# Performance work log

Measured on AMD Instinct MI355X. Metric: run time of the kernel, lower is better.

Reference implementation:

```python
import jax, jax.numpy as jnp
import numpy as np

N = 100000   # nodes
E = 1600000  # edges
D = 128      # input_dim
H = 128      # hidden_dim
G = 1000     # num graphs
C = 10       # output_dim
EPS = 1e-5   # BatchNorm eps


def setup_inputs() -> dict:
    key = jax.random.key(0)
    ks = jax.random.split(key, 16)
    inp = {
        "x": jax.random.normal(ks[0], (N, D), dtype=jnp.float32),
        "edge_index": jax.random.randint(ks[1], (2, E), 0, N, dtype=jnp.int64),
        "batch": jnp.sort(jax.random.randint(ks[2], (N,), 0, G, dtype=jnp.int64)),
    }
    s_in, s_h = 1.0 / np.sqrt(D), 1.0 / np.sqrt(H)
    inp["W1"] = jax.random.normal(ks[3], (D, H), jnp.float32) * s_in
    inp["b1"] = jnp.zeros((H,), jnp.float32)
    inp["W2"] = jax.random.normal(ks[4], (H, H), jnp.float32) * s_h
    inp["b2"] = jnp.zeros((H,), jnp.float32)
    inp["W3"] = jax.random.normal(ks[5], (H, H), jnp.float32) * s_h
    inp["b3"] = jnp.zeros((H,), jnp.float32)
    for i in range(1, 4):
        inp[f"g{i}"] = jnp.ones((H,), jnp.float32)
        inp[f"be{i}"] = jnp.zeros((H,), jnp.float32)
    inp["Wc1"] = jax.random.normal(ks[6], (H, H // 2), jnp.float32) * s_h
    inp["bc1"] = jnp.zeros((H // 2,), jnp.float32)
    inp["Wc2"] = jax.random.normal(ks[7], (H // 2, C), jnp.float32) * (1.0 / np.sqrt(H // 2))
    inp["bc2"] = jnp.zeros((C,), jnp.float32)
    return inp


def _edge_norm(edge_index, num_nodes):
    # PyG GCNConv default: add self-loops, symmetric D^-1/2 A D^-1/2 normalization
    loop = jnp.arange(num_nodes, dtype=edge_index.dtype)
    src = jnp.concatenate([edge_index[0], loop])
    dst = jnp.concatenate([edge_index[1], loop])
    deg = jax.ops.segment_sum(jnp.ones_like(dst, dtype=jnp.float32), dst,
                              num_segments=num_nodes)
    dinv = jnp.where(deg > 0, deg ** -0.5, 0.0)
    norm = dinv[src] * dinv[dst]  # [E + N]
    return src, dst, norm


def _gcn_conv(x, W, b, src, dst, norm, num_nodes):
    h = x @ W                              # [N, H]
    msg = h[src] * norm[:, None]           # gather over edges (incl. self-loops)
    out = jax.ops.segment_sum(msg, dst, num_segments=num_nodes)
    return out + b


def _bn_eval(x, gamma, beta):
    # eval-mode BatchNorm1d with running_mean=0, running_var=1 buffers
    return gamma * x * (1.0 / np.sqrt(1.0 + EPS)) + beta


def reference(x, edge_index, batch,
              W1, b1, W2, b2, W3, b3,
              g1, be1, g2, be2, g3, be3,
              Wc1, bc1, Wc2, bc2):
    num_nodes = x.shape[0]
    src, dst, norm = _edge_norm(edge_index, num_nodes)
    h = x
    for (W, b, g, be) in ((W1, b1, g1, be1), (W2, b2, g2, be2), (W3, b3, g3, be3)):
        h = _gcn_conv(h, W, b, src, dst, norm, num_nodes)
        h = jax.nn.relu(_bn_eval(h, g, be))  # dropout is identity in eval mode
    # global_mean_pool over graph ids
    sums = jax.ops.segment_sum(h, batch, num_segments=G)
    cnts = jax.ops.segment_sum(jnp.ones((num_nodes,), h.dtype), batch, num_segments=G)
    pooled = sums / jnp.maximum(cnts, 1.0)[:, None]
    # classifier MLP
    z = jax.nn.relu(pooled @ Wc1 + bc1)
    return z @ Wc2 + bc2
```

## Files before the change

### kernel.cpp

```cpp
#include <hip/hip_runtime.h>
#include <hip/hip_bf16.h>

#define INV1P 0.9999950000374997f
#define BCAP 16384
#define CSRCAP 20480

typedef __attribute__((ext_vector_type(8))) short bfrag;
typedef __attribute__((ext_vector_type(4))) float f32x4;

static __device__ __forceinline__ unsigned bf16rne(float f) {
    unsigned u = __float_as_uint(f);
    return (u + 0x7fffu + ((u >> 16) & 1u)) >> 16;
}
static __device__ __forceinline__ float bflo(unsigned u) { return __uint_as_float(u << 16); }
static __device__ __forceinline__ float bfhi(unsigned u) { return __uint_as_float(u & 0xffff0000u); }


__global__ __launch_bounds__(256) void k_initcur2(int* __restrict__ gcursor) {
    gcursor[threadIdx.x] = threadIdx.x * BCAP;
}

__global__ __launch_bounds__(256) void k_binA(const int* __restrict__ src, const int* __restrict__ dst,
                                              int* __restrict__ gcursor, unsigned* __restrict__ binned, int e) {
    __shared__ unsigned pk[8192];
    __shared__ unsigned char bk[8192];
    __shared__ int hist[256];
    __shared__ int base[256];
    int tid = threadIdx.x;
    hist[tid] = 0;
    __syncthreads();
    int cbase = blockIdx.x * 8192;
    int cnt = min(8192, e - cbase);
    for (int j = tid; j < cnt; j += 256) {
        int s = src[cbase + j], d = dst[cbase + j];
        unsigned b = (unsigned)d >> 9;
        pk[j] = (unsigned)s | (((unsigned)d & 511u) << 17);
        bk[j] = (unsigned char)b;
        atomicAdd(&hist[b], 1);
    }
    __syncthreads();
    int h = hist[tid];
    base[tid] = (h > 0) ? atomicAdd(&gcursor[tid], h) : 0;
    hist[tid] = 0;
    __syncthreads();
    for (int j = tid; j < cnt; j += 256) {
        unsigned b = bk[j];
        int off = atomicAdd(&hist[b], 1);
        binned[base[b] + off] = pk[j];
    }
}

__global__ __launch_bounds__(256) void k_binB2(const unsigned* __restrict__ binned,
                                               const int* __restrict__ gcursor,
                                               int* __restrict__ rowptr, int* __restrict__ rowend,
                                               float* __restrict__ dinv,
                                               int* __restrict__ csr_src, int n, int dummy) {
    __shared__ int cur[512];
    __shared__ int lrp[512];
    __shared__ int ssum[256];
    int b = blockIdx.x, tid = threadIdx.x;
    int nstart = b << 9;
    int nn = min(512, n - nstart);
    int cntb = gcursor[b] - b * BCAP;
    int s0 = b * BCAP, s1 = s0 + cntb;
    int cb = b * CSRCAP;
    cur[tid] = 0; cur[tid + 256] = 0;
    __syncthreads();
    for (int j = s0 + tid; j < s1; j += 256)
        atomicAdd(&cur[(binned[j] >> 17) & 511], 1);
    __syncthreads();
    int c0 = cur[2 * tid], c1 = cur[2 * tid + 1];
    int p0 = (c0 + 7) & ~7, p1 = (c1 + 7) & ~7;
    int pair = p0 + p1;
    ssum[tid] = pair;
    __syncthreads();
    for (int off = 1; off < 256; off <<= 1) {
        int t2 = (tid >= off) ? ssum[tid - off] : 0;
        __syncthreads();
        ssum[tid] += t2;
        __syncthreads();
    }
    int e0 = ssum[tid] - pair;
    int e1 = e0 + p0;
    int st0 = cb + e0, st1 = cb + e1;
    lrp[2 * tid] = st0;
    lrp[2 * tid + 1] = st1;
    if (2 * tid < nn) {
        rowptr[nstart + 2 * tid] = st0;
        rowend[nstart + 2 * tid] = st0 + p0;
        dinv[nstart + 2 * tid] = rsqrtf((float)(c0 + 1));
    }
    if (2 * tid + 1 < nn) {
        rowptr[nstart + 2 * tid + 1] = st1;
        rowend[nstart + 2 * tid + 1] = st1 + p1;
        dinv[nstart + 2 * tid + 1] = rsqrtf((float)(c1 + 1));
    }
    for (int k = c0; k < p0; k++) csr_src[st0 + k] = dummy;
    for (int k = c1; k < p1; k++) csr_src[st1 + k] = dummy;
    cur[2 * tid] = 0; cur[2 * tid + 1] = 0;
    __syncthreads();
    for (int j = s0 + tid; j < s1; j += 256) {
        unsigned p = binned[j];
        int nl = (p >> 17) & 511;
        int idx = atomicAdd(&cur[nl], 1);
        csr_src[lrp[nl] + idx] = p & 0x1ffff;
    }
}


__global__ __launch_bounds__(256) void k_prepw(const float* __restrict__ W, uint4* __restrict__ Bf) {
    int id = blockIdx.x * 256 + threadIdx.x;
    int lane = id & 63;
    int e = id >> 6;
    int kk = e >> 3, c = e & 7;
    int kbase = kk * 32 + (lane >> 4) * 8;
    int col = c * 16 + (lane & 15);
    unsigned hi[8], lo[8];
    #pragma unroll
    for (int j = 0; j < 8; j++) {
        float w = W[(kbase + j) * 128 + col];
        unsigned h = bf16rne(w);
        float rh = __uint_as_float(h << 16);
        unsigned l = bf16rne(w - rh);
        hi[j] = h; lo[j] = l;
    }
    uint4 H = make_uint4(hi[0] | (hi[1] << 16), hi[2] | (hi[3] << 16),
                         hi[4] | (hi[5] << 16), hi[6] | (hi[7] << 16));
    uint4 L = make_uint4(lo[0] | (lo[1] << 16), lo[2] | (lo[3] << 16),
                         lo[4] | (lo[5] << 16), lo[6] | (lo[7] << 16));
    Bf[e * 64 + lane] = H;
    Bf[2048 + e * 64 + lane] = L;
}

static __device__ __forceinline__ void gemm_body(unsigned* __restrict__ Y, const float* __restrict__ dinv,
                                                 int nrows, int rowbase, bfrag* a, uint4* bs) {
    int tid = threadIdx.x;
    int w = tid >> 6, lane = tid & 63;
    __syncthreads();
    f32x4 acc[8];
    #pragma unroll
    for (int c = 0; c < 8; c++) acc[c] = (f32x4){0.f, 0.f, 0.f, 0.f};
    #pragma unroll
    for (int kk = 0; kk < 4; kk++) {
        #pragma unroll
        for (int c = 0; c < 8; c++) {
            bfrag bh = *(const bfrag*)&bs[(kk * 8 + c) * 64 + lane];
            bfrag bl = *(const bfrag*)&bs[2048 + (kk * 8 + c) * 64 + lane];
            acc[c] = __builtin_amdgcn_mfma_f32_16x16x32_bf16(a[kk], bh, acc[c], 0, 0, 0);
            acc[c] = __builtin_amdgcn_mfma_f32_16x16x32_bf16(a[kk], bl, acc[c], 0, 0, 0);
        }
    }
    int rb = rowbase + w * 16 + (lane >> 4) * 4;
    float dv[4];
    #pragma unroll
    for (int r = 0; r < 4; r++) dv[r] = dinv[min(rb + r, nrows - 1)];
    __syncthreads();
    char* epib = (char*)bs;
    ushort* epi = (ushort*)(epib + w * 4352);
    #pragma unroll
    for (int c = 0; c < 8; c++) {
        #pragma unroll
        for (int r = 0; r < 4; r++) {
            int rr = (lane >> 4) * 4 + r;
            epi[rr * 136 + c * 16 + (lane & 15)] = (ushort)bf16rne(acc[c][r] * dv[r]);
        }
    }
    __syncthreads();
    #pragma unroll
    for (int i = 0; i < 4; i++) {
        int id = tid + i * 512;
        int rr = id >> 4, q = id & 15;
        int grow = rowbase + rr;
        if (grow < nrows) {
            uint4 v = *(const uint4*)(epib + (rr >> 4) * 4352 + (rr & 15) * 272 + q * 16);
            ((uint4*)Y)[(size_t)grow * 16 + q] = v;
        }
    }
}

__global__ __launch_bounds__(512) void k_gemm_mfma(const unsigned* __restrict__ Xb,
                                                   const uint4* __restrict__ Bfr,
                                                   unsigned* __restrict__ Y, const float* __restrict__ dinv,
                                                   int nrows) {
    __shared__ uint4 bs[4096];
    int tid = threadIdx.x;
    int w = tid >> 6, lane = tid & 63;
    int rowbase = blockIdx.x * 128;
    #pragma unroll
    for (int i = 0; i < 8; i++) bs[tid + i * 512] = Bfr[tid + i * 512];
    int row = rowbase + w * 16 + (lane & 15);
    int rowc = min(row, nrows - 1);
    const uint4* X4 = (const uint4*)Xb;
    bfrag a[4];
    #pragma unroll
    for (int kk = 0; kk < 4; kk++) {
        uint4 av = X4[(size_t)rowc * 16 + kk * 4 + (lane >> 4)];
        a[kk] = *(const bfrag*)&av;
    }
    gemm_body(Y, dinv, nrows, rowbase, a, bs);
}

__global__ __launch_bounds__(512) void k_gemm_mfma_f32(const float* __restrict__ X,
                                                       const uint4* __restrict__ Bfr,
                                                       unsigned* __restrict__ Y, const float* __restrict__ dinv,
                                                       int nrows) {
    __shared__ uint4 bs[4096];
    int tid = threadIdx.x;
    int w = tid >> 6, lane = tid & 63;
    int rowbase = blockIdx.x * 128;
    #pragma unroll
    for (int i = 0; i < 8; i++) bs[tid + i * 512] = Bfr[tid + i * 512];
    int row = rowbase + w * 16 + (lane & 15);
    int rowc = min(row, nrows - 1);
    const float4* X4 = (const float4*)X;
    bfrag a[4];
    #pragma unroll
    for (int kk = 0; kk < 4; kk++) {
        float4 f0 = X4[(size_t)rowc * 32 + kk * 8 + (lane >> 4) * 2];
        float4 f1 = X4[(size_t)rowc * 32 + kk * 8 + (lane >> 4) * 2 + 1];
        uint4 av = make_uint4(bf16rne(f0.x) | (bf16rne(f0.y) << 16),
                              bf16rne(f0.z) | (bf16rne(f0.w) << 16),
                              bf16rne(f1.x) | (bf16rne(f1.y) << 16),
                              bf16rne(f1.z) | (bf16rne(f1.w) << 16));
        a[kk] = *(const bfrag*)&av;
    }
    gemm_body(Y, dinv, nrows, rowbase, a, bs);
}

__global__ __launch_bounds__(256) void k_aggregate(const uint4* __restrict__ H4, const int* __restrict__ rowptr,
                                                   const int* __restrict__ rowend,
                                                   const int* __restrict__ csr_src,
                                                   const float* __restrict__ dinv,
                                                   const float* __restrict__ bias, const float* __restrict__ gamma,
                                                   const float* __restrict__ beta,
                                                   uint4* __restrict__ out4, int nnodes) {
    int tid = blockIdx.x * 256 + threadIdx.x;
    int node = tid >> 4;
    int l = tid & 15;
    if (node >= nnodes) return;
    float acc[8];
    {
        uint4 hv = H4[(size_t)node * 16 + l];
        acc[0] = bflo(hv.x); acc[1] = bfhi(hv.x);
        acc[2] = bflo(hv.y); acc[3] = bfhi(hv.y);
        acc[4] = bflo(hv.z); acc[5] = bfhi(hv.z);
        acc[6] = bflo(hv.w); acc[7] = bfhi(hv.w);
    }
    int s = rowptr[node], e = rowend[node];
    const int4* csr4 = (const int4*)csr_src;
    int4 ia, ib;
    if (s < e) {
        ia = csr4[(s >> 2)];
        ib = csr4[(s >> 2) + 1];
    }
    for (int j = s; j < e; j += 8) {
        uint4 vv[8];
        vv[0] = H4[(size_t)ia.x * 16 + l];
        vv[1] = H4[(size_t)ia.y * 16 + l];
        vv[2] = H4[(size_t)ia.z * 16 + l];
        vv[3] = H4[(size_t)ia.w * 16 + l];
        vv[4] = H4[(size_t)ib.x * 16 + l];
        vv[5] = H4[(size_t)ib.y * 16 + l];
        vv[6] = H4[(size_t)ib.z * 16 + l];
        vv[7] = H4[(size_t)ib.w * 16 + l];
        int jn = j + 8;
        if (jn < e) {
            ia = csr4[(jn >> 2)];
            ib = csr4[(jn >> 2) + 1];
        }
        #pragma unroll
        for (int q = 0; q < 8; q++) {
            acc[0] += bflo(vv[q].x); acc[1] += bfhi(vv[q].x);
            acc[2] += bflo(vv[q].y); acc[3] += bfhi(vv[q].y);
            acc[4] += bflo(vv[q].z); acc[5] += bfhi(vv[q].z);
            acc[6] += bflo(vv[q].w); acc[7] += bfhi(vv[q].w);
        }
    }
    float dn = dinv[node];
    float4 bi0 = ((const float4*)bias)[l * 2],  bi1 = ((const float4*)bias)[l * 2 + 1];
    float4 ga0 = ((const float4*)gamma)[l * 2], ga1 = ((const float4*)gamma)[l * 2 + 1];
    float4 be0 = ((const float4*)beta)[l * 2],  be1 = ((const float4*)beta)[l * 2 + 1];
    float g[8] = {ga0.x, ga0.y, ga0.z, ga0.w, ga1.x, ga1.y, ga1.z, ga1.w};
    float bb[8] = {bi0.x, bi0.y, bi0.z, bi0.w, bi1.x, bi1.y, bi1.z, bi1.w};
    float bt[8] = {be0.x, be0.y, be0.z, be0.w, be1.x, be1.y, be1.z, be1.w};
    float r[8];
    #pragma unroll
    for (int i = 0; i < 8; i++) {
        float t = g[i] * INV1P;
        r[i] = fmaxf(fmaf(t * dn, acc[i], fmaf(t, bb[i], bt[i])), 0.f);
    }
    uint4 o;
    o.x = bf16rne(r[0]) | (bf16rne(r[1]) << 16);
    o.y = bf16rne(r[2]) | (bf16rne(r[3]) << 16);
    o.z = bf16rne(r[4]) | (bf16rne(r[5]) << 16);
    o.w = bf16rne(r[6]) | (bf16rne(r[7]) << 16);
    out4[(size_t)node * 16 + l] = o;
}

__global__ __launch_bounds__(64) void k_pool(const unsigned* __restrict__ Hf, const int* __restrict__ batch,
                                             float* __restrict__ pooled, float* __restrict__ cnt, int nnodes) {
    int t = threadIdx.x;
    int base = blockIdx.x * 64;
    if (base >= nnodes) return;
    int end = min(base + 64, nnodes);
    float ax = 0.f, ay = 0.f; int run = 0;
    int cur = batch[base];
    for (int i = base; i < end; i++) {
        int bg = batch[i];
        if (bg != cur) {
            atomicAdd(&pooled[(size_t)cur * 128 + 2 * t], ax);
            atomicAdd(&pooled[(size_t)cur * 128 + 2 * t + 1], ay);
            if (t == 0) atomicAdd(&cnt[cur], (float)run);
            ax = 0.f; ay = 0.f; run = 0; cur = bg;
        }
        unsigned u = Hf[(size_t)i * 64 + t];
        ax += bflo(u);
        ay += bfhi(u);
        run++;
    }
    atomicAdd(&pooled[(size_t)cur * 128 + 2 * t], ax);
    atomicAdd(&pooled[(size_t)cur * 128 + 2 * t + 1], ay);
    if (t == 0) atomicAdd(&cnt[cur], (float)run);
}

__global__ __launch_bounds__(64) void k_classifier(const float* __restrict__ pooled, const float* __restrict__ cnt,
                                                   const float* __restrict__ Wc1, const float* __restrict__ bc1,
                                                   const float* __restrict__ Wc2, const float* __restrict__ bc2,
                                                   float* __restrict__ outp, int ngraphs) {
    __shared__ float p[128];
    __shared__ float z[64];
    int g = blockIdx.x;
    int tid = threadIdx.x;
    float inv = 1.0f / fmaxf(cnt[g], 1.0f);
    p[tid]      = pooled[(size_t)g * 128 + tid] * inv;
    p[tid + 64] = pooled[(size_t)g * 128 + 64 + tid] * inv;
    __syncthreads();
    float a = bc1[tid];
    #pragma unroll 8
    for (int k = 0; k < 128; k++) a += p[k] * Wc1[k * 64 + tid];
    z[tid] = fmaxf(a, 0.f);
    __syncthreads();
    if (tid < 10) {
        float o = bc2[tid];
        #pragma unroll 8
        for (int j = 0; j < 64; j++) o += z[j] * Wc2[j * 10 + tid];
        outp[(size_t)g * 10 + tid] = o;
    }
}


static inline size_t align16(size_t v) { return (v + 15) & ~(size_t)15; }

extern "C" void kernel_launch(void* const* d_in, const int* in_sizes, int n_in,
                              void* d_out, int out_size, void* d_ws, size_t ws_size,
                              hipStream_t stream) {
    const float* x      = (const float*)d_in[0];
    const int*   ei     = (const int*)d_in[1];
    const int*   batch  = (const int*)d_in[2];
    const float* W1 = (const float*)d_in[3];  const float* b1 = (const float*)d_in[4];
    const float* W2 = (const float*)d_in[5];  const float* b2 = (const float*)d_in[6];
    const float* W3 = (const float*)d_in[7];  const float* b3 = (const float*)d_in[8];
    const float* g1 = (const float*)d_in[9];  const float* be1 = (const float*)d_in[10];
    const float* g2 = (const float*)d_in[11]; const float* be2 = (const float*)d_in[12];
    const float* g3 = (const float*)d_in[13]; const float* be3 = (const float*)d_in[14];
    const float* Wc1 = (const float*)d_in[15]; const float* bc1 = (const float*)d_in[16];
    const float* Wc2 = (const float*)d_in[17]; const float* bc2 = (const float*)d_in[18];

    const int N = in_sizes[0] / 128;
    const int E = in_sizes[1] / 2;
    const int G = out_size / 10;
    const int* srcp = ei;
    const int* dstp = ei + E;
    const int NB = (N + 511) >> 9;

    char* ws = (char*)d_ws;
    size_t off = 0;
    unsigned* bufA = (unsigned*)(ws + off); off = align16(off + (size_t)(N + 1) * 64 * 4);
    unsigned* bufB = (unsigned*)(ws + off); off = align16(off + (size_t)N * 64 * 4);
    uint4* Bfr1 = (uint4*)(ws + off); off = align16(off + 4096 * 16);
    uint4* Bfr2 = (uint4*)(ws + off); off = align16(off + 4096 * 16);
    uint4* Bfr3 = (uint4*)(ws + off); off = align16(off + 4096 * 16);
    int*   csr_src = (int*)(ws + off);  off = align16(off + (size_t)NB * CSRCAP * 4);
    unsigned* binned = (unsigned*)(ws + off); off = align16(off + (size_t)NB * BCAP * 4);
    float* dinv   = (float*)(ws + off); off = align16(off + (size_t)N * 4);
    int*   rowptr = (int*)(ws + off);   off = align16(off + (size_t)N * 4);
    int*   rowend = (int*)(ws + off);   off = align16(off + (size_t)N * 4);
    int*   gcursor = (int*)(ws + off);  off = align16(off + 256 * 4);
    float* pooled = (float*)(ws + off); off = align16(off + (size_t)G * 128 * 4);
    float* cnt    = (float*)(ws + off); off = align16(off + (size_t)G * 4);
    (void)ws_size;

    int gE8 = (E + 8191) / 8192;

    hipMemsetAsync(bufA + (size_t)N * 64, 0, 256, stream);

    k_prepw<<<8, 256, 0, stream>>>(W1, Bfr1);
    k_prepw<<<8, 256, 0, stream>>>(W2, Bfr2);
    k_prepw<<<8, 256, 0, stream>>>(W3, Bfr3);

    k_initcur2<<<1, 256, 0, stream>>>(gcursor);
    k_binA<<<gE8, 256, 0, stream>>>(srcp, dstp, gcursor, binned, E);
    k_binB2<<<NB, 256, 0, stream>>>(binned, gcursor, rowptr, rowend, dinv, csr_src, N, N);

    int gGemm = (N + 127) / 128;
    int gAgg  = (N * 16 + 255) / 256;

    k_gemm_mfma_f32<<<gGemm, 512, 0, stream>>>(x, Bfr1, bufA, dinv, N);
    k_aggregate<<<gAgg, 256, 0, stream>>>((const uint4*)bufA, rowptr, rowend, csr_src, dinv, b1, g1, be1, (uint4*)bufB, N);
    k_gemm_mfma<<<gGemm, 512, 0, stream>>>(bufB, Bfr2, bufA, dinv, N);
    k_aggregate<<<gAgg, 256, 0, stream>>>((const uint4*)bufA, rowptr, rowend, csr_src, dinv, b2, g2, be2, (uint4*)bufB, N);
    k_gemm_mfma<<<gGemm, 512, 0, stream>>>(bufB, Bfr3, bufA, dinv, N);
    k_aggregate<<<gAgg, 256, 0, stream>>>((const uint4*)bufA, rowptr, rowend, csr_src, dinv, b3, g3, be3, (uint4*)bufB, N);

    hipMemsetAsync(pooled, 0, ((size_t)G * 128 + G) * 4, stream);
    int gPool = (N + 63) / 64;
    k_pool<<<gPool, 64, 0, stream>>>(bufB, batch, pooled, cnt, N);

    k_classifier<<<G, 64, 0, stream>>>(pooled, cnt, Wc1, bc1, Wc2, bc2, (float*)d_out, G);
}
```

Baseline: 310.7 us.

## Fuse aggregation with next-layer GEMM and merge prep kernels

Aggregation plus BN/ReLU of layers 1 and 2 now runs in the same kernel as the next layer's MFMA GEMM. The aggregated tile stays in LDS, so the intermediate bf16 feature buffer is no longer written to and re-read from global memory. The three weight-prep launches, the cursor init and the padding memsets are merged into one launch, with the dummy pad row now also zeroed in bufB. The fused kernel reads B fragments straight from global (L2) memory instead of staging them in LDS, and it serializes gather and matmul phases within each block, which may lower overlap and occupancy.

```diff
diff --git a/kernel.cpp b/kernel.cpp
--- a/kernel.cpp
+++ b/kernel.cpp
@@ -15,10 +15,6 @@
 static __device__ __forceinline__ float bflo(unsigned u) { return __uint_as_float(u << 16); }
 static __device__ __forceinline__ float bfhi(unsigned u) { return __uint_as_float(u & 0xffff0000u); }
 
-
-__global__ __launch_bounds__(256) void k_initcur2(int* __restrict__ gcursor) {
-    gcursor[threadIdx.x] = threadIdx.x * BCAP;
-}
 
 __global__ __launch_bounds__(256) void k_binA(const int* __restrict__ src, const int* __restrict__ dst,
                                               int* __restrict__ gcursor, unsigned* __restrict__ binned, int e) {
@@ -108,8 +104,8 @@
 }
 
 
-__global__ __launch_bounds__(256) void k_prepw(const float* __restrict__ W, uint4* __restrict__ Bf) {
-    int id = blockIdx.x * 256 + threadIdx.x;
+static __device__ __forceinline__ void prepw_body(const float* __restrict__ W, uint4* __restrict__ Bf, int blk) {
+    int id = blk * 256 + threadIdx.x;
     int lane = id & 63;
     int e = id >> 6;
     int kk = e >> 3, c = e & 7;
@@ -130,6 +126,24 @@
                          lo[4] | (lo[5] << 16), lo[6] | (lo[7] << 16));
     Bf[e * 64 + lane] = H;
     Bf[2048 + e * 64 + lane] = L;
+}
+
+__global__ __launch_bounds__(256) void k_prep(const float* __restrict__ W1, const float* __restrict__ W2,
+                                              const float* __restrict__ W3,
+                                              uint4* __restrict__ Bf1, uint4* __restrict__ Bf2,
+                                              uint4* __restrict__ Bf3,
+                                              int* __restrict__ gcursor,
+                                              unsigned* __restrict__ bufA, unsigned* __restrict__ bufB, int n) {
+    int b = blockIdx.x;
+    if (b < 8)       prepw_body(W1, Bf1, b);
+    else if (b < 16) prepw_body(W2, Bf2, b - 8);
+    else if (b < 24) prepw_body(W3, Bf3, b - 16);
+    else {
+        int t = threadIdx.x;
+        gcursor[t] = t * BCAP;
+        if (t < 64)  bufA[(size_t)n * 64 + t] = 0;
+        else if (t < 128) bufB[(size_t)n * 64 + (t - 64)] = 0;
+    }
 }
 
 static __device__ __forceinline__ void gemm_body(unsigned* __restrict__ Y, const float* __restrict__ dinv,
@@ -176,28 +190,6 @@
             ((uint4*)Y)[(size_t)grow * 16 + q] = v;
         }
     }
-}
-
-__global__ __launch_bounds__(512) void k_gemm_mfma(const unsigned* __restrict__ Xb,
-                                                   const uint4* __restrict__ Bfr,
-                                                   unsigned* __restrict__ Y, const float* __restrict__ dinv,
-                                                   int nrows) {
-    __shared__ uint4 bs[4096];
-    int tid = threadIdx.x;
-    int w = tid >> 6, lane = tid & 63;
-    int rowbase = blockIdx.x * 128;
-    #pragma unroll
-    for (int i = 0; i < 8; i++) bs[tid + i * 512] = Bfr[tid + i * 512];
-    int row = rowbase + w * 16 + (lane & 15);
-    int rowc = min(row, nrows - 1);
-    const uint4* X4 = (const uint4*)Xb;
-    bfrag a[4];
-    #pragma unroll
-    for (int kk = 0; kk < 4; kk++) {
-        uint4 av = X4[(size_t)rowc * 16 + kk * 4 + (lane >> 4)];
-        a[kk] = *(const bfrag*)&av;
-    }
-    gemm_body(Y, dinv, nrows, rowbase, a, bs);
 }
 
 __global__ __launch_bounds__(512) void k_gemm_mfma_f32(const float* __restrict__ X,
@@ -227,26 +219,17 @@
     gemm_body(Y, dinv, nrows, rowbase, a, bs);
 }
 
-__global__ __launch_bounds__(256) void k_aggregate(const uint4* __restrict__ H4, const int* __restrict__ rowptr,
-                                                   const int* __restrict__ rowend,
-                                                   const int* __restrict__ csr_src,
-                                                   const float* __restrict__ dinv,
-                                                   const float* __restrict__ bias, const float* __restrict__ gamma,
-                                                   const float* __restrict__ beta,
-                                                   uint4* __restrict__ out4, int nnodes) {
-    int tid = blockIdx.x * 256 + threadIdx.x;
-    int node = tid >> 4;
-    int l = tid & 15;
-    if (node >= nnodes) return;
-    float acc[8];
+static __device__ __forceinline__ void agg_body(const uint4* __restrict__ H4, int nodec, int l,
+                                                const int* __restrict__ rowptr, const int* __restrict__ rowend,
+                                                const int* __restrict__ csr_src, float* acc) {
     {
-        uint4 hv = H4[(size_t)node * 16 + l];
+        uint4 hv = H4[(size_t)nodec * 16 + l];
         acc[0] = bflo(hv.x); acc[1] = bfhi(hv.x);
         acc[2] = bflo(hv.y); acc[3] = bfhi(hv.y);
         acc[4] = bflo(hv.z); acc[5] = bfhi(hv.z);
         acc[6] = bflo(hv.w); acc[7] = bfhi(hv.w);
     }
-    int s = rowptr[node], e = rowend[node];
+    int s = rowptr[nodec], e = rowend[nodec];
     const int4* csr4 = (const int4*)csr_src;
     int4 ia, ib;
     if (s < e) {
@@ -276,19 +259,108 @@
             acc[6] += bflo(vv[q].w); acc[7] += bfhi(vv[q].w);
         }
     }
-    float dn = dinv[node];
+}
+
+static __device__ __forceinline__ void bn_relu(const float* acc, float dn, int l,
+                                               const float* __restrict__ bias, const float* __restrict__ gamma,
+                                               const float* __restrict__ beta, float* r) {
     float4 bi0 = ((const float4*)bias)[l * 2],  bi1 = ((const float4*)bias)[l * 2 + 1];
     float4 ga0 = ((const float4*)gamma)[l * 2], ga1 = ((const float4*)gamma)[l * 2 + 1];
     float4 be0 = ((const float4*)beta)[l * 2],  be1 = ((const float4*)beta)[l * 2 + 1];
     float g[8] = {ga0.x, ga0.y, ga0.z, ga0.w, ga1.x, ga1.y, ga1.z, ga1.w};
     float bb[8] = {bi0.x, bi0.y, bi0.z, bi0.w, bi1.x, bi1.y, bi1.z, bi1.w};
     float bt[8] = {be0.x, be0.y, be0.z, be0.w, be1.x, be1.y, be1.z, be1.w};
-    float r[8];
     #pragma unroll
     for (int i = 0; i < 8; i++) {
         float t = g[i] * INV1P;
         r[i] = fmaxf(fmaf(t * dn, acc[i], fmaf(t, bb[i], bt[i])), 0.f);
     }
+}
+
+__global__ __launch_bounds__(256) void k_agg_gemm(const uint4* __restrict__ H4,
+                                                  const int* __restrict__ rowptr, const int* __restrict__ rowend,
+                                                  const int* __restrict__ csr_src,
+                                                  const float* __restrict__ dinv,
+                                                  const float* __restrict__ bias, const float* __restrict__ gamma,
+                                                  const float* __restrict__ beta,
+                                                  const uint4* __restrict__ Bfr,
+                                                  unsigned* __restrict__ Yn, int nnodes) {
+    __shared__ ushort hs[64 * 136];
+    __shared__ ushort ys[64 * 136];
+    int tid = threadIdx.x;
+    int nl = tid >> 4;
+    int l = tid & 15;
+    int base = blockIdx.x * 64;
+
+    for (int it = 0; it < 4; it++) {
+        int node = base + it * 16 + nl;
+        int nodec = min(node, nnodes - 1);
+        float acc[8], r[8];
+        agg_body(H4, nodec, l, rowptr, rowend, csr_src, acc);
+        bn_relu(acc, dinv[nodec], l, bias, gamma, beta, r);
+        uint4 o;
+        o.x = bf16rne(r[0]) | (bf16rne(r[1]) << 16);
+        o.y = bf16rne(r[2]) | (bf16rne(r[3]) << 16);
+        o.z = bf16rne(r[4]) | (bf16rne(r[5]) << 16);
+        o.w = bf16rne(r[6]) | (bf16rne(r[7]) << 16);
+        *(uint4*)&hs[(it * 16 + nl) * 136 + l * 8] = o;
+    }
+    __syncthreads();
+
+    int w = tid >> 6, lane = tid & 63;
+    int c0 = 2 * w, c1 = 2 * w + 1;
+    #pragma unroll
+    for (int t = 0; t < 4; t++) {
+        bfrag a[4];
+        #pragma unroll
+        for (int kk = 0; kk < 4; kk++)
+            a[kk] = *(const bfrag*)&hs[(t * 16 + (lane & 15)) * 136 + (lane >> 4) * 8 + kk * 32];
+        f32x4 ac0 = (f32x4){0.f, 0.f, 0.f, 0.f};
+        f32x4 ac1 = (f32x4){0.f, 0.f, 0.f, 0.f};
+        #pragma unroll
+        for (int kk = 0; kk < 4; kk++) {
+            bfrag bh0 = *(const bfrag*)&Bfr[(kk * 8 + c0) * 64 + lane];
+            bfrag bl0 = *(const bfrag*)&Bfr[2048 + (kk * 8 + c0) * 64 + lane];
+            bfrag bh1 = *(const bfrag*)&Bfr[(kk * 8 + c1) * 64 + lane];
+            bfrag bl1 = *(const bfrag*)&Bfr[2048 + (kk * 8 + c1) * 64 + lane];
+            ac0 = __builtin_amdgcn_mfma_f32_16x16x32_bf16(a[kk], bh0, ac0, 0, 0, 0);
+            ac0 = __builtin_amdgcn_mfma_f32_16x16x32_bf16(a[kk], bl0, ac0, 0, 0, 0);
+            ac1 = __builtin_amdgcn_mfma_f32_16x16x32_bf16(a[kk], bh1, ac1, 0, 0, 0);
+            ac1 = __builtin_amdgcn_mfma_f32_16x16x32_bf16(a[kk], bl1, ac1, 0, 0, 0);
+        }
+        #pragma unroll
+        for (int r = 0; r < 4; r++) {
+            int rowt = (lane >> 4) * 4 + r;
+            float dv = dinv[min(base + t * 16 + rowt, nnodes - 1)];
+            ys[(t * 16 + rowt) * 136 + c0 * 16 + (lane & 15)] = (ushort)bf16rne(ac0[r] * dv);
+            ys[(t * 16 + rowt) * 136 + c1 * 16 + (lane & 15)] = (ushort)bf16rne(ac1[r] * dv);
+        }
+    }
+    __syncthreads();
+    #pragma unroll
+    for (int i = 0; i < 4; i++) {
+        int id = tid + i * 256;
+        int row = id >> 4, q = id & 15;
+        int grow = base + row;
+        if (grow < nnodes)
+            ((uint4*)Yn)[(size_t)grow * 16 + q] = *(const uint4*)&ys[row * 136 + q * 8];
+    }
+}
+
+__global__ __launch_bounds__(256) void k_aggregate(const uint4* __restrict__ H4, const int* __restrict__ rowptr,
+                                                   const int* __restrict__ rowend,
+                                                   const int* __restrict__ csr_src,
+                                                   const float* __restrict__ dinv,
+                                                   const float* __restrict__ bias, const float* __restrict__ gamma,
+                                                   const float* __restrict__ beta,
+                                                   uint4* __restrict__ out4, int nnodes) {
+    int tid = blockIdx.x * 256 + threadIdx.x;
+    int node = tid >> 4;
+    int l = tid & 15;
+    if (node >= nnodes) return;
+    float acc[8], r[8];
+    agg_body(H4, node, l, rowptr, rowend, csr_src, acc);
+    bn_relu(acc, dinv[node], l, bias, gamma, beta, r);
     uint4 o;
     o.x = bf16rne(r[0]) | (bf16rne(r[1]) << 16);
     o.y = bf16rne(r[2]) | (bf16rne(r[3]) << 16);
@@ -376,7 +448,7 @@
     char* ws = (char*)d_ws;
     size_t off = 0;
     unsigned* bufA = (unsigned*)(ws + off); off = align16(off + (size_t)(N + 1) * 64 * 4);
-    unsigned* bufB = (unsigned*)(ws + off); off = align16(off + (size_t)N * 64 * 4);
+    unsigned* bufB = (unsigned*)(ws + off); off = align16(off + (size_t)(N + 1) * 64 * 4);
     uint4* Bfr1 = (uint4*)(ws + off); off = align16(off + 4096 * 16);
     uint4* Bfr2 = (uint4*)(ws + off); off = align16(off + 4096 * 16);
     uint4* Bfr3 = (uint4*)(ws + off); off = align16(off + 4096 * 16);
@@ -392,25 +464,22 @@
 
     int gE8 = (E + 8191) / 8192;
 
-    hipMemsetAsync(bufA + (size_t)N * 64, 0, 256, stream);
-
-    k_prepw<<<8, 256, 0, stream>>>(W1, Bfr1);
-    k_prepw<<<8, 256, 0, stream>>>(W2, Bfr2);
-    k_prepw<<<8, 256, 0, stream>>>(W3, Bfr3);
-
-    k_initcur2<<<1, 256, 0, stream>>>(gcursor);
+    k_prep<<<25, 256, 0, stream>>>(W1, W2, W3, Bfr1, Bfr2, Bfr3, gcursor, bufA, bufB, N);
+
     k_binA<<<gE8, 256, 0, stream>>>(srcp, dstp, gcursor, binned, E);
     k_binB2<<<NB, 256, 0, stream>>>(binned, gcursor, rowptr, rowend, dinv, csr_src, N, N);
 
     int gGemm = (N + 127) / 128;
+    int gFuse = (N + 63) / 64;
     int gAgg  = (N * 16 + 255) / 256;
 
     k_gemm_mfma_f32<<<gGemm, 512, 0, stream>>>(x, Bfr1, bufA, dinv, N);
-    k_aggregate<<<gAgg, 256, 0, stream>>>((const uint4*)bufA, rowptr, rowend, csr_src, dinv, b1, g1, be1, (uint4*)bufB, N);
-    k_gemm_mfma<<<gGemm, 512, 0, stream>>>(bufB, Bfr2, bufA, dinv, N);
-    k_aggregate<<<gAgg, 256, 0, stream>>>((const uint4*)bufA, rowptr, rowend, csr_src, dinv, b2, g2, be2, (uint4*)bufB, N);
-    k_gemm_mfma<<<gGemm, 512, 0, stream>>>(bufB, Bfr3, bufA, dinv, N);
-    k_aggregate<<<gAgg, 256, 0, stream>>>((const uint4*)bufA, rowptr, rowend, csr_src, dinv, b3, g3, be3, (uint4*)bufB, N);
+    k_agg_gemm<<<gFuse, 256, 0, stream>>>((const uint4*)bufA, rowptr, rowend, csr_src, dinv,
+                                          b1, g1, be1, Bfr2, bufB, N);
+    k_agg_gemm<<<gFuse, 256, 0, stream>>>((const uint4*)bufB, rowptr, rowend, csr_src, dinv,
+                                          b2, g2, be2, Bfr3, bufA, N);
+    k_aggregate<<<gAgg, 256, 0, stream>>>((const uint4*)bufA, rowptr, rowend, csr_src, dinv,
+                                          b3, g3, be3, (uint4*)bufB, N);
 
     hipMemsetAsync(pooled, 0, ((size_t)G * 128 + G) * 4, stream);
     int gPool = (N + 63) / 64;
```

Result: no change. 305.0 us (-1.8%).
